# Kernel tuning notes

Measured on AMD Instinct MI355X. Metric: run time of the kernel, lower is better.

The kernel has to match this reference:

```python
import jax, jax.numpy as jnp
import numpy as np

DIM = 256
GRID = 5


def setup_inputs() -> dict:
    key = jax.random.key(0)
    kx, kw = jax.random.split(key)
    x = jax.random.normal(kx, (32, 2048, DIM), dtype=jnp.float32)
    scale = 1.0 / (np.sqrt(DIM) * np.sqrt(GRID))
    fourier_weight = jax.random.normal(kw, (2, DIM, DIM, GRID), dtype=jnp.float32) * scale
    bias = jnp.zeros((DIM,), dtype=jnp.float32)
    return {"x": x, "fourier_weight": fourier_weight, "bias": bias}


def reference(x, fourier_weight, bias):
    D = bias.shape[0]
    G = fourier_weight.shape[-1]
    out_shape = x.shape[:-1] + (D,)
    xf = x.reshape(-1, D)                                  # (N, D)
    k = jnp.arange(1, G + 1, dtype=x.dtype)                # (G,)
    arg = xf[:, :, None] * k                               # (N, D, G)
    # y[n,o] = sum_{d,g} cos(k_g x[n,d]) W[0,o,d,g] + sin(k_g x[n,d]) W[1,o,d,g] + b[o]
    y = jnp.einsum('ndg,odg->no', jnp.cos(arg), fourier_weight[0])
    y = y + jnp.einsum('ndg,odg->no', jnp.sin(arg), fourier_weight[1])
    y = y + bias
    return y.reshape(out_shape)
```

## Files before the change

kernel.cpp:

```cpp
#include <hip/hip_runtime.h>
#include <hip/hip_bf16.h>
#include <stdint.h>

#define DIM 256
#define GRID_G 5
#define KTOT (DIM * GRID_G * 2)
#define BM 128
#define BN 256
#define BK 64
#define NTHREADS 512

typedef float f32x4 __attribute__((ext_vector_type(4)));
typedef short bf16x8 __attribute__((ext_vector_type(8)));

static __device__ __forceinline__ uint32_t f2bf_bits(float v) {
    uint32_t u = __float_as_uint(v);
    return (u + 0x7FFFu + ((u >> 16) & 1u)) >> 16;
}

static __device__ __forceinline__ void gload_lds16(const void* g, void* l) {
    __builtin_amdgcn_global_load_lds(
        (const __attribute__((address_space(1))) void*)g,
        (__attribute__((address_space(3))) void*)l, 16, 0, 0);
}

__global__ void wtransform(const float* __restrict__ W, uint16_t* __restrict__ Wb) {
    int idx = blockIdx.x * blockDim.x + threadIdx.x;
    if (idx >= DIM * KTOT) return;
    int o = idx / KTOT;
    int k = idx - o * KTOT;
    int g = k >> 9;
    int r = k & 511;
    int d = r >> 1;
    int s = r & 1;
    float w = W[(((s * DIM + o) * DIM + d) * GRID_G) + g];
    Wb[idx] = (uint16_t)f2bf_bits(w);
}

__global__ __launch_bounds__(NTHREADS, 4)
void fourier_gemm(const float* __restrict__ x, const uint16_t* __restrict__ Wb,
                  const float* __restrict__ bias, float* __restrict__ out) {
    __shared__ __align__(16) short As[BM * BK];
    __shared__ __align__(16) short Bs[BN * BK];

    const int tid  = threadIdx.x;
    const int lane = tid & 63;
    const int wave = tid >> 6;
    const int wrow = wave >> 2;
    const int wcol = wave & 3;
    const int row0 = blockIdx.x * BM;

    f32x4 acc[4][4];
#pragma unroll
    for (int m = 0; m < 4; ++m)
#pragma unroll
        for (int n = 0; n < 4; ++n)
            acc[m][n] = (f32x4){0.f, 0.f, 0.f, 0.f};

    const int sd = tid & 31;
    const int sn = tid >> 5;

    const int q16 = (lane >> 4) << 4;

    for (int c = 0; c < KTOT / BK; ++c) {
        const int g  = c >> 3;
        const int d0 = (c & 7) * 32;
        const float kg = (float)(g + 1);

        {
            const char* wbb = (const char*)Wb + (size_t)c * 128;
#pragma unroll
            for (int i = 0; i < 4; ++i) {
                int f   = tid * 16 + i * 8192;
                int o   = f >> 7;
                int col = f & 127;
                int scol = col ^ ((o & 7) << 4);
                gload_lds16(wbb + (size_t)o * (KTOT * 2) + scol, (char*)Bs + f);
            }
        }

        {
#pragma unroll
            for (int i = 0; i < 8; ++i) {
                int n = sn + i * 16;
                float xv = x[(size_t)(row0 + n) * DIM + (d0 + sd)];
                float a  = kg * xv;
                float sv = __sinf(a);
                float cv = __cosf(a);
                uint32_t pk = (f2bf_bits(sv) << 16) | f2bf_bits(cv);
                int boff = (n * 128 + sd * 4) ^ ((n & 7) << 4);
                *(uint32_t*)((char*)As + boff) = pk;
            }
        }

        __syncthreads();

#pragma unroll
        for (int ks = 0; ks < 2; ++ks) {
            bf16x8 af[4], bfr[4];
#pragma unroll
            for (int m = 0; m < 4; ++m) {
                int r = wrow * 64 + m * 16 + (lane & 15);
                int off = (r * 128 + ks * 64 + q16) ^ ((r & 7) << 4);
                af[m] = *(const bf16x8*)((const char*)As + off);
            }
#pragma unroll
            for (int nf = 0; nf < 4; ++nf) {
                int o = wcol * 64 + nf * 16 + (lane & 15);
                int off = (o * 128 + ks * 64 + q16) ^ ((o & 7) << 4);
                bfr[nf] = *(const bf16x8*)((const char*)Bs + off);
            }
#pragma unroll
            for (int m = 0; m < 4; ++m)
#pragma unroll
                for (int nf = 0; nf < 4; ++nf)
                    acc[m][nf] = __builtin_amdgcn_mfma_f32_16x16x32_bf16(
                        af[m], bfr[nf], acc[m][nf], 0, 0, 0);
        }

        __syncthreads();
    }

#pragma unroll
    for (int m = 0; m < 4; ++m) {
        int rbase = row0 + wrow * 64 + m * 16 + ((lane >> 4) << 2);
#pragma unroll
        for (int nf = 0; nf < 4; ++nf) {
            int ocol = wcol * 64 + nf * 16 + (lane & 15);
            float b = bias[ocol];
#pragma unroll
            for (int r = 0; r < 4; ++r) {
                out[(size_t)(rbase + r) * DIM + ocol] = acc[m][nf][r] + b;
            }
        }
    }
}

extern "C" void kernel_launch(void* const* d_in, const int* in_sizes, int n_in,
                              void* d_out, int out_size, void* d_ws, size_t ws_size,
                              hipStream_t stream) {
    const float* x    = (const float*)d_in[0];
    const float* W    = (const float*)d_in[1];
    const float* bias = (const float*)d_in[2];
    float* out        = (float*)d_out;
    uint16_t* Wb      = (uint16_t*)d_ws;

    int rows = in_sizes[0] / DIM;
    int wtot = DIM * KTOT;

    hipLaunchKernelGGL(wtransform, dim3((wtot + 255) / 256), dim3(256), 0, stream, W, Wb);
    hipLaunchKernelGGL(fourier_gemm, dim3(rows / BM), dim3(NTHREADS), 0, stream,
                       x, Wb, bias, out);
}
```

Measured before the change: 236.2 us.

## Double-buffer LDS tiles, enlarge row tile, use hardware sin/cos with packed bf16 convert

Double-buffers the A and B LDS tiles so the next chunk's weight loads and x loads are issued before the MFMA work on the current chunk, with the trig feature generation for the next chunk done after the MFMAs. Doubles the row tile to 256 per block, so each wave computes 8x4 MFMA fragments and more reuse comes from each B tile. Trig is done with raw v_sin/v_cos on pre-scaled inputs and packed bf16 conversion instead of __sinf/__cosf plus manual rounding. The cost is a larger LDS footprint and more registers, dropping to 2 blocks per CU with half as many blocks overall, and the hardware trig may lose accuracy for large arguments.

```diff
diff --git a/kernel.cpp b/kernel.cpp
--- a/kernel.cpp
+++ b/kernel.cpp
@@ -5,10 +5,13 @@
 #define DIM 256
 #define GRID_G 5
 #define KTOT (DIM * GRID_G * 2)
-#define BM 128
+#define BM 256
 #define BN 256
 #define BK 64
 #define NTHREADS 512
+#define NCHUNK (KTOT / BK)
+#define AS_SH (BM * BK)
+#define BS_SH (BN * BK)
 
 typedef float f32x4 __attribute__((ext_vector_type(4)));
 typedef short bf16x8 __attribute__((ext_vector_type(8)));
@@ -37,11 +40,11 @@
     Wb[idx] = (uint16_t)f2bf_bits(w);
 }
 
-__global__ __launch_bounds__(NTHREADS, 4)
+__global__ __launch_bounds__(NTHREADS, 2)
 void fourier_gemm(const float* __restrict__ x, const uint16_t* __restrict__ Wb,
                   const float* __restrict__ bias, float* __restrict__ out) {
-    __shared__ __align__(16) short As[BM * BK];
-    __shared__ __align__(16) short Bs[BN * BK];
+    __shared__ __align__(16) short As[2 * AS_SH];
+    __shared__ __align__(16) short Bs[2 * BS_SH];
 
     const int tid  = threadIdx.x;
     const int lane = tid & 63;
@@ -49,85 +52,121 @@
     const int wrow = wave >> 2;
     const int wcol = wave & 3;
     const int row0 = blockIdx.x * BM;
+    const int q16  = (lane >> 4) << 4;
 
-    f32x4 acc[4][4];
+    f32x4 acc[8][4];
 #pragma unroll
-    for (int m = 0; m < 4; ++m)
+    for (int m = 0; m < 8; ++m)
 #pragma unroll
         for (int n = 0; n < 4; ++n)
             acc[m][n] = (f32x4){0.f, 0.f, 0.f, 0.f};
 
-    const int sd = tid & 31;
-    const int sn = tid >> 5;
+    const int sd2 = tid & 15;
+    const int sn  = tid >> 4;
 
-    const int q16 = (lane >> 4) << 4;
+    float2 xq[8];
 
-    for (int c = 0; c < KTOT / BK; ++c) {
-        const int g  = c >> 3;
-        const int d0 = (c & 7) * 32;
-        const float kg = (float)(g + 1);
+#define STAGE_B(cc, buf)                                                      \
+    {                                                                         \
+        const char* wbb = (const char*)Wb + (size_t)(cc) * 128;               \
+        char* dst = (char*)(Bs + (buf) * BS_SH);                              \
+        _Pragma("unroll")                                                     \
+        for (int i = 0; i < 4; ++i) {                                         \
+            int f = tid * 16 + i * 8192;                                      \
+            int o = f >> 7;                                                   \
+            int col = f & 127;                                                \
+            int scol = col ^ ((o & 7) << 4);                                  \
+            gload_lds16(wbb + (size_t)o * (KTOT * 2) + scol, dst + f);        \
+        }                                                                     \
+    }
 
-        {
-            const char* wbb = (const char*)Wb + (size_t)c * 128;
-#pragma unroll
-            for (int i = 0; i < 4; ++i) {
-                int f   = tid * 16 + i * 8192;
-                int o   = f >> 7;
-                int col = f & 127;
-                int scol = col ^ ((o & 7) << 4);
-                gload_lds16(wbb + (size_t)o * (KTOT * 2) + scol, (char*)Bs + f);
-            }
+#define LOAD_X(cc)                                                            \
+    {                                                                         \
+        int d0 = ((cc) & 7) * 32;                                             \
+        _Pragma("unroll")                                                     \
+        for (int i = 0; i < 8; ++i) {                                         \
+            int n = sn + i * 32;                                              \
+            xq[i] = *(const float2*)&x[(size_t)(row0 + n) * DIM + d0 + 2 * sd2]; \
+        }                                                                     \
+    }
+
+#define TRIG_WRITE(cc, buf)                                                   \
+    {                                                                         \
+        float kgrev = (float)(((cc) >> 3) + 1) * 0.15915494309189535f;        \
+        char* abase = (char*)(As + (buf) * AS_SH);                            \
+        _Pragma("unroll")                                                     \
+        for (int i = 0; i < 8; ++i) {                                         \
+            int n = sn + i * 32;                                              \
+            float r0 = xq[i].x * kgrev;                                       \
+            float r1 = xq[i].y * kgrev;                                       \
+            float s0, c0, s1, c1;                                             \
+            asm("v_sin_f32 %0, %1" : "=v"(s0) : "v"(r0));                     \
+            asm("v_cos_f32 %0, %1" : "=v"(c0) : "v"(r0));                     \
+            asm("v_sin_f32 %0, %1" : "=v"(s1) : "v"(r1));                     \
+            asm("v_cos_f32 %0, %1" : "=v"(c1) : "v"(r1));                     \
+            uint32_t p0, p1;                                                  \
+            asm("v_cvt_pk_bf16_f32 %0, %1, %2" : "=v"(p0) : "v"(c0), "v"(s0));\
+            asm("v_cvt_pk_bf16_f32 %0, %1, %2" : "=v"(p1) : "v"(c1), "v"(s1));\
+            int boff = (n * 128 + sd2 * 8) ^ ((n & 7) << 4);                  \
+            uint64_t pk = ((uint64_t)p1 << 32) | (uint64_t)p0;                \
+            *(uint64_t*)(abase + boff) = pk;                                  \
+        }                                                                     \
+    }
+
+    STAGE_B(0, 0);
+    LOAD_X(0);
+    TRIG_WRITE(0, 0);
+    __syncthreads();
+
+    for (int c = 0; c < NCHUNK; ++c) {
+        const int cur = c & 1;
+        const int nxt = cur ^ 1;
+
+        if (c + 1 < NCHUNK) {
+            STAGE_B(c + 1, nxt);
+            LOAD_X(c + 1);
         }
 
-        {
-#pragma unroll
-            for (int i = 0; i < 8; ++i) {
-                int n = sn + i * 16;
-                float xv = x[(size_t)(row0 + n) * DIM + (d0 + sd)];
-                float a  = kg * xv;
-                float sv = __sinf(a);
-                float cv = __cosf(a);
-                uint32_t pk = (f2bf_bits(sv) << 16) | f2bf_bits(cv);
-                int boff = (n * 128 + sd * 4) ^ ((n & 7) << 4);
-                *(uint32_t*)((char*)As + boff) = pk;
-            }
-        }
-
-        __syncthreads();
+        const char* Ac = (const char*)(As + cur * AS_SH);
+        const char* Bc = (const char*)(Bs + cur * BS_SH);
 
 #pragma unroll
         for (int ks = 0; ks < 2; ++ks) {
-            bf16x8 af[4], bfr[4];
+            bf16x8 af[8], bfr[4];
 #pragma unroll
-            for (int m = 0; m < 4; ++m) {
-                int r = wrow * 64 + m * 16 + (lane & 15);
+            for (int m = 0; m < 8; ++m) {
+                int r = wrow * 128 + m * 16 + (lane & 15);
                 int off = (r * 128 + ks * 64 + q16) ^ ((r & 7) << 4);
-                af[m] = *(const bf16x8*)((const char*)As + off);
+                af[m] = *(const bf16x8*)(Ac + off);
             }
 #pragma unroll
             for (int nf = 0; nf < 4; ++nf) {
                 int o = wcol * 64 + nf * 16 + (lane & 15);
                 int off = (o * 128 + ks * 64 + q16) ^ ((o & 7) << 4);
-                bfr[nf] = *(const bf16x8*)((const char*)Bs + off);
+                bfr[nf] = *(const bf16x8*)(Bc + off);
             }
 #pragma unroll
-            for (int m = 0; m < 4; ++m)
+            for (int m = 0; m < 8; ++m)
 #pragma unroll
                 for (int nf = 0; nf < 4; ++nf)
                     acc[m][nf] = __builtin_amdgcn_mfma_f32_16x16x32_bf16(
                         af[m], bfr[nf], acc[m][nf], 0, 0, 0);
         }
 
+        if (c + 1 < NCHUNK) {
+            TRIG_WRITE(c + 1, nxt);
+        }
+
         __syncthreads();
     }
 
 #pragma unroll
-    for (int m = 0; m < 4; ++m) {
-        int rbase = row0 + wrow * 64 + m * 16 + ((lane >> 4) << 2);
+    for (int nf = 0; nf < 4; ++nf) {
+        int ocol = wcol * 64 + nf * 16 + (lane & 15);
+        float b = bias[ocol];
 #pragma unroll
-        for (int nf = 0; nf < 4; ++nf) {
-            int ocol = wcol * 64 + nf * 16 + (lane & 15);
-            float b = bias[ocol];
+        for (int m = 0; m < 8; ++m) {
+            int rbase = row0 + wrow * 128 + m * 16 + ((lane >> 4) << 2);
 #pragma unroll
             for (int r = 0; r < 4; ++r) {
                 out[(size_t)(rbase + r) * DIM + ocol] = acc[m][nf][r] + b;
```

Result: faster. 200.5 us (-15.1%).
